# Kernel optimization log

Hardware: AMD Instinct MI355X
Metric: run time of the kernel (lower is better)

The kernel has to match this reference:

```python
import jax, jax.numpy as jnp
import numpy as np

D = 4096
B = 2
S = 2048


def setup_inputs() -> dict:
    key = jax.random.key(0)
    k1, k2, k3, k4 = jax.random.split(key, 4)
    x = jax.random.normal(k1, (B, S, D), dtype=jnp.float32)
    # 2-bit symmetric quantized codes stored as uint8 in torch; torch's
    # clamp(-1,1).to(uint8) wraps -1 -> 255, so codes span {0,1,255}-like
    # values. We draw the full uint8 range for a representative baseline.
    q_int = jax.random.randint(k2, (D, D), 0, 256, dtype=jnp.int32)
    # per-channel positive scales (small, like 2-bit scales: |w|max / 1)
    scale = jax.random.uniform(k3, (D,), dtype=jnp.float32) * 0.01 + 1e-4
    # symmetric quantization -> zero_point = 0 per channel (int buffer)
    zero_point = jnp.zeros((D,), dtype=jnp.int32)
    bias = jax.random.normal(k4, (D,), dtype=jnp.float32) * 0.02
    return {"x": x, "q_int": q_int, "scale": scale,
            "zero_point": zero_point, "bias": bias}


def reference(x, q_int, scale, zero_point, bias):
    # Faithful to FFQLinear.forward:
    #   weight = (q_int.float() - zero_point) * scale
    # NOTE: no unsqueeze(-1) here (unlike pack time), so scale/zp broadcast
    # over the LAST (column) axis of the [d, d] code matrix.
    zp = zero_point.astype(jnp.float32)
    W = (q_int.astype(jnp.float32) - zp[None, :]) * scale[None, :]  # [D, D]
    b, s, d = x.shape
    # F.linear(x2d, W.t(), bias) == x2d @ W + bias
    out = jnp.einsum('bsd,dk->bsk', x, W) + bias  # [B, S, D]
    return out
```

## Files before the change

kernel.cpp:

```cpp
#include <hip/hip_runtime.h>
#include <stdint.h>

typedef unsigned short u16;
typedef __attribute__((ext_vector_type(8))) short short8;
typedef __attribute__((ext_vector_type(4))) float f32x4;

#define KD 4096

typedef const __attribute__((address_space(1))) void* gas1_t;
typedef __attribute__((address_space(3))) void* las3_t;

__device__ __forceinline__ void g2l16(const void* g, void* l) {
  __builtin_amdgcn_global_load_lds((gas1_t)g, (las3_t)l, 16, 0, 0);
}

__device__ __forceinline__ u16 f2bf(float f) {
  uint32_t u = __float_as_uint(f);
  return (u16)((u + 0x7FFFu + ((u >> 16) & 1u)) >> 16);
}

__global__ void cvt_x(const float4* __restrict__ x, uint2* __restrict__ xb) {
  int gid = blockIdx.x * 256 + threadIdx.x;
  float4 f = x[gid];
  union { u16 u[4]; uint2 v; } o;
  o.u[0] = f2bf(f.x); o.u[1] = f2bf(f.y);
  o.u[2] = f2bf(f.z); o.u[3] = f2bf(f.w);
  xb[gid] = o.v;
}

__global__ void cvt_q(const int* __restrict__ q, const int* __restrict__ zp,
                      u16* __restrict__ qt) {
  __shared__ u16 Lt[64][66];
  const int n0 = blockIdx.x * 64;
  const int k0 = blockIdx.y * 64;
  const int nc = threadIdx.x & 15;
  const int kr = threadIdx.x >> 4;

  int z[4];
#pragma unroll
  for (int c = 0; c < 4; ++c) z[c] = zp[n0 + nc * 4 + c];

#pragma unroll
  for (int p = 0; p < 4; ++p) {
    int k = p * 16 + kr;
    int4 v = *(const int4*)(q + (int64_t)(k0 + k) * KD + n0 + nc * 4);
    Lt[k][nc * 4 + 0] = f2bf((float)(v.x - z[0]));
    Lt[k][nc * 4 + 1] = f2bf((float)(v.y - z[1]));
    Lt[k][nc * 4 + 2] = f2bf((float)(v.z - z[2]));
    Lt[k][nc * 4 + 3] = f2bf((float)(v.w - z[3]));
  }
  __syncthreads();

  const int kq = threadIdx.x & 7;
  const int nn = threadIdx.x >> 3;
#pragma unroll
  for (int p = 0; p < 2; ++p) {
    int n = nn + p * 32;
    union { u16 u[8]; uint4 v; } o;
#pragma unroll
    for (int i = 0; i < 8; ++i) o.u[i] = Lt[kq * 8 + i][n];
    *(uint4*)(qt + (int64_t)(n0 + n) * KD + k0 + kq * 8) = o.v;
  }
}

__global__ __launch_bounds__(512, 2)
void gemm8(const u16* __restrict__ A, const u16* __restrict__ Bt,
           const float* __restrict__ scale, const float* __restrict__ bias,
           float* __restrict__ C) {
  __shared__ u16 lds[65536];

  const int tid = threadIdx.x;
  const int orig = blockIdx.x;
  const int lid = (orig & 7) * 32 + (orig >> 3);
  const int bm0 = (lid >> 4) * 256;
  const int bn0 = (lid & 15) * 256;

  const int lane = tid & 63;
  const int w = tid >> 6;
  const int wr = w >> 2;
  const int wc = w & 3;
  const int l15 = lane & 15;
  const int q4 = lane >> 4;
  const int l7 = l15 & 7;

  const int rl = tid >> 3;
  const int csw = (tid & 7) ^ (rl & 7);
  const u16* gA = A + (int64_t)(bm0 + rl) * KD + csw * 8;
  const u16* gB = Bt + (int64_t)(bn0 + rl) * KD + csw * 8;

#define STA(b, qq, kt) g2l16(gA + (int64_t)(qq) * 64 * KD + (kt), &lds[(b) * 32768 + (qq) * 4096 + tid * 8])
#define STB(b, qq, kt) g2l16(gB + (int64_t)(qq) * 64 * KD + (kt), &lds[16384 + (b) * 32768 + (qq) * 4096 + tid * 8])

#define RD_A(mh)                                                              \
  do {                                                                        \
    _Pragma("unroll") for (int m = 0; m < 4; ++m) {                           \
      const int row = wr * 128 + (mh) * 64 + m * 16 + l15;                    \
      _Pragma("unroll") for (int kk = 0; kk < 2; ++kk)                        \
        ar[m][kk] = *(const short8*)&Ab[row * 64 + (((kk * 4 + q4) ^ l7) * 8)]; \
    }                                                                         \
  } while (0)

#define RD_B(nn0)                                                             \
  do {                                                                        \
    _Pragma("unroll") for (int n = 0; n < 2; ++n) {                           \
      const int col = wc * 64 + ((nn0) + n) * 16 + l15;                       \
      _Pragma("unroll") for (int kk = 0; kk < 2; ++kk)                        \
        br[(nn0) + n][kk] = *(const short8*)&Bb[col * 64 + (((kk * 4 + q4) ^ l7) * 8)]; \
    }                                                                         \
  } while (0)

#define MFMA_Q(mb, nn0)                                                       \
  do {                                                                        \
    __builtin_amdgcn_s_setprio(1);                                            \
    _Pragma("unroll") for (int m = 0; m < 4; ++m)                             \
      _Pragma("unroll") for (int n = 0; n < 2; ++n)                           \
        _Pragma("unroll") for (int kk = 0; kk < 2; ++kk)                      \
          acc[(mb) + m][(nn0) + n] = __builtin_amdgcn_mfma_f32_16x16x32_bf16( \
              ar[m][kk], br[(nn0) + n][kk], acc[(mb) + m][(nn0) + n], 0, 0, 0); \
    __builtin_amdgcn_s_setprio(0);                                            \
  } while (0)

#define LGKM0 asm volatile("s_waitcnt lgkmcnt(0)" ::: "memory")
#define BAR __builtin_amdgcn_s_barrier()

  f32x4 acc[8][4];
#pragma unroll
  for (int m = 0; m < 8; ++m)
#pragma unroll
    for (int n = 0; n < 4; ++n) acc[m][n] = (f32x4)(0.f);

  short8 ar[4][2], br[4][2];

  STB(0, 0, 0); STB(0, 1, 0); STB(0, 2, 0); STB(0, 3, 0);
  STA(0, 0, 0); STA(0, 2, 0); STA(0, 1, 0); STA(0, 3, 0);
  asm volatile("s_waitcnt vmcnt(2)" ::: "memory");
  BAR;

  int cur = 0;
  for (int t = 0; t < 63; ++t) {
    const int ktn = (t + 1) * 64;
    const u16* __restrict__ Ab = &lds[cur * 32768];
    const u16* __restrict__ Bb = &lds[16384 + cur * 32768];
    const int nb = cur ^ 1;

    RD_A(0);
    RD_B(0);
    STB(nb, 0, ktn); STB(nb, 1, ktn);
    BAR; LGKM0;
    MFMA_Q(0, 0);
    BAR;

    RD_B(2);
    STB(nb, 2, ktn); STB(nb, 3, ktn);
    asm volatile("s_waitcnt vmcnt(4)" ::: "memory");
    BAR; LGKM0;
    MFMA_Q(0, 2);
    BAR;

    RD_A(1);
    STA(nb, 0, ktn); STA(nb, 2, ktn);
    BAR; LGKM0;
    MFMA_Q(4, 0);
    BAR;

    STA(nb, 1, ktn); STA(nb, 3, ktn);
    asm volatile("s_waitcnt vmcnt(2)" ::: "memory");
    BAR; LGKM0;
    MFMA_Q(4, 2);
    BAR;

    cur ^= 1;
  }

  {
    const u16* __restrict__ Ab = &lds[cur * 32768];
    const u16* __restrict__ Bb = &lds[16384 + cur * 32768];
    RD_A(0);
    RD_B(0);
    BAR; LGKM0;
    MFMA_Q(0, 0);
    BAR;

    RD_B(2);
    asm volatile("s_waitcnt vmcnt(0)" ::: "memory");
    BAR; LGKM0;
    MFMA_Q(0, 2);
    BAR;

    RD_A(1);
    BAR; LGKM0;
    MFMA_Q(4, 0);
    BAR;

    MFMA_Q(4, 2);
  }

  const int r4 = q4 * 4;
#pragma unroll
  for (int n = 0; n < 4; ++n) {
    const int col = bn0 + wc * 64 + n * 16 + l15;
    const float sc = scale[col];
    const float bs = bias[col];
#pragma unroll
    for (int mi = 0; mi < 8; ++mi) {
      const int row = bm0 + wr * 128 + mi * 16 + r4;
#pragma unroll
      for (int j = 0; j < 4; ++j)
        C[(int64_t)(row + j) * KD + col] = acc[mi][n][j] * sc + bs;
    }
  }
}

extern "C" void kernel_launch(void* const* d_in, const int* in_sizes, int n_in,
                              void* d_out, int out_size, void* d_ws, size_t ws_size,
                              hipStream_t stream) {
  const float* x = (const float*)d_in[0];
  const int* q = (const int*)d_in[1];
  const float* scale = (const float*)d_in[2];
  const int* zp = (const int*)d_in[3];
  const float* bias = (const float*)d_in[4];
  float* out = (float*)d_out;

  u16* Xb = (u16*)d_ws;
  u16* Qt = Xb + (size_t)4096 * 4096;

  cvt_x<<<16384, 256, 0, stream>>>((const float4*)x, (uint2*)Xb);

  dim3 gq(4096 / 64, 4096 / 64);
  cvt_q<<<gq, 256, 0, stream>>>(q, zp, Qt);

  gemm8<<<256, 512, 0, stream>>>(Xb, Qt, scale, bias, out);
}
```

Baseline: 294.9 us.

## Fuse conversion kernels and simplify GEMM loop to two barriers per k-step

The two preprocessing kernels (x to bf16, and the transpose-convert of the quantized weights) are merged into one launch. Block ranges select the role, and the weight transpose now packs pairs of k rows into 32-bit LDS words so the readback needs fewer LDS reads. In the GEMM main loop all eight global-to-LDS prefetches for the next tile are issued at once behind a single barrier pair, replacing the four sub-phases that each had barriers. This cuts synchronisation and launch overhead. The trade-offs are coarser overlap between loads and MFMAs and a dependence on the vmcnt(8) accounting being correct.

```diff
diff --git a/kernel.cpp b/kernel.cpp
--- a/kernel.cpp
+++ b/kernel.cpp
@@ -19,35 +19,42 @@
   return (u16)((u + 0x7FFFu + ((u >> 16) & 1u)) >> 16);
 }
 
-__global__ void cvt_x(const float4* __restrict__ x, uint2* __restrict__ xb) {
-  int gid = blockIdx.x * 256 + threadIdx.x;
-  float4 f = x[gid];
-  union { u16 u[4]; uint2 v; } o;
-  o.u[0] = f2bf(f.x); o.u[1] = f2bf(f.y);
-  o.u[2] = f2bf(f.z); o.u[3] = f2bf(f.w);
-  xb[gid] = o.v;
-}
-
-__global__ void cvt_q(const int* __restrict__ q, const int* __restrict__ zp,
-                      u16* __restrict__ qt) {
-  __shared__ u16 Lt[64][66];
-  const int n0 = blockIdx.x * 64;
-  const int k0 = blockIdx.y * 64;
+__global__ __launch_bounds__(256)
+void cvt_fused(const float4* __restrict__ x, const int* __restrict__ q,
+               const int* __restrict__ zp, uint2* __restrict__ xb,
+               u16* __restrict__ qt) {
+  const int b = blockIdx.x;
+  if (b >= 4096) {
+    int gid = (b - 4096) * 256 + threadIdx.x;
+    float4 f = x[gid];
+    union { u16 u[4]; uint2 v; } o;
+    o.u[0] = f2bf(f.x); o.u[1] = f2bf(f.y);
+    o.u[2] = f2bf(f.z); o.u[3] = f2bf(f.w);
+    xb[gid] = o.v;
+    return;
+  }
+  __shared__ uint32_t P[32][68];
+  const int n0 = (b & 63) * 64;
+  const int k0 = (b >> 6) * 64;
   const int nc = threadIdx.x & 15;
   const int kr = threadIdx.x >> 4;
 
   int z[4];
 #pragma unroll
-  for (int c = 0; c < 4; ++c) z[c] = zp[n0 + nc * 4 + c];
-
-#pragma unroll
-  for (int p = 0; p < 4; ++p) {
-    int k = p * 16 + kr;
-    int4 v = *(const int4*)(q + (int64_t)(k0 + k) * KD + n0 + nc * 4);
-    Lt[k][nc * 4 + 0] = f2bf((float)(v.x - z[0]));
-    Lt[k][nc * 4 + 1] = f2bf((float)(v.y - z[1]));
-    Lt[k][nc * 4 + 2] = f2bf((float)(v.z - z[2]));
-    Lt[k][nc * 4 + 3] = f2bf((float)(v.w - z[3]));
+  for (int j = 0; j < 4; ++j) z[j] = zp[n0 + nc * 4 + j];
+
+#pragma unroll
+  for (int s = 0; s < 2; ++s) {
+    const int kp = kr + s * 16;
+    const int64_t rb = (int64_t)(k0 + kp * 2) * KD + n0 + nc * 4;
+    int4 r0 = *(const int4*)(q + rb);
+    int4 r1 = *(const int4*)(q + rb + KD);
+    uint4 w;
+    w.x = (uint32_t)f2bf((float)(r0.x - z[0])) | ((uint32_t)f2bf((float)(r1.x - z[0])) << 16);
+    w.y = (uint32_t)f2bf((float)(r0.y - z[1])) | ((uint32_t)f2bf((float)(r1.y - z[1])) << 16);
+    w.z = (uint32_t)f2bf((float)(r0.z - z[2])) | ((uint32_t)f2bf((float)(r1.z - z[2])) << 16);
+    w.w = (uint32_t)f2bf((float)(r0.w - z[3])) | ((uint32_t)f2bf((float)(r1.w - z[3])) << 16);
+    *(uint4*)&P[kp][nc * 4] = w;
   }
   __syncthreads();
 
@@ -55,11 +62,13 @@
   const int nn = threadIdx.x >> 3;
 #pragma unroll
   for (int p = 0; p < 2; ++p) {
-    int n = nn + p * 32;
-    union { u16 u[8]; uint4 v; } o;
-#pragma unroll
-    for (int i = 0; i < 8; ++i) o.u[i] = Lt[kq * 8 + i][n];
-    *(uint4*)(qt + (int64_t)(n0 + n) * KD + k0 + kq * 8) = o.v;
+    const int n = nn + p * 32;
+    uint4 v;
+    v.x = P[kq * 4 + 0][n];
+    v.y = P[kq * 4 + 1][n];
+    v.z = P[kq * 4 + 2][n];
+    v.w = P[kq * 4 + 3][n];
+    *(uint4*)(qt + (int64_t)(n0 + n) * KD + k0 + kq * 8) = v;
   }
 }
 
@@ -88,8 +97,8 @@
   const u16* gA = A + (int64_t)(bm0 + rl) * KD + csw * 8;
   const u16* gB = Bt + (int64_t)(bn0 + rl) * KD + csw * 8;
 
-#define STA(b, qq, kt) g2l16(gA + (int64_t)(qq) * 64 * KD + (kt), &lds[(b) * 32768 + (qq) * 4096 + tid * 8])
-#define STB(b, qq, kt) g2l16(gB + (int64_t)(qq) * 64 * KD + (kt), &lds[16384 + (b) * 32768 + (qq) * 4096 + tid * 8])
+#define STA(b_, qq, kt) g2l16(gA + (int64_t)(qq) * 64 * KD + (kt), &lds[(b_) * 32768 + (qq) * 4096 + tid * 8])
+#define STB(b_, qq, kt) g2l16(gB + (int64_t)(qq) * 64 * KD + (kt), &lds[16384 + (b_) * 32768 + (qq) * 4096 + tid * 8])
 
 #define RD_A(mh)                                                              \
   do {                                                                        \
@@ -120,8 +129,11 @@
     __builtin_amdgcn_s_setprio(0);                                            \
   } while (0)
 
-#define LGKM0 asm volatile("s_waitcnt lgkmcnt(0)" ::: "memory")
 #define BAR __builtin_amdgcn_s_barrier()
+#define SCHED0 __builtin_amdgcn_sched_barrier(0)
+#define CFENCE asm volatile("" ::: "memory")
+#define VMC8 asm volatile("s_waitcnt vmcnt(8)" ::: "memory")
+#define VMC0 asm volatile("s_waitcnt vmcnt(0)" ::: "memory")
 
   f32x4 acc[8][4];
 #pragma unroll
@@ -132,9 +144,7 @@
   short8 ar[4][2], br[4][2];
 
   STB(0, 0, 0); STB(0, 1, 0); STB(0, 2, 0); STB(0, 3, 0);
-  STA(0, 0, 0); STA(0, 2, 0); STA(0, 1, 0); STA(0, 3, 0);
-  asm volatile("s_waitcnt vmcnt(2)" ::: "memory");
-  BAR;
+  STA(0, 0, 0); STA(0, 1, 0); STA(0, 2, 0); STA(0, 3, 0);
 
   int cur = 0;
   for (int t = 0; t < 63; ++t) {
@@ -143,31 +153,22 @@
     const u16* __restrict__ Bb = &lds[16384 + cur * 32768];
     const int nb = cur ^ 1;
 
+    SCHED0; CFENCE;
+    BAR;
+    STB(nb, 0, ktn); STB(nb, 1, ktn); STB(nb, 2, ktn); STB(nb, 3, ktn);
+    STA(nb, 0, ktn); STA(nb, 1, ktn); STA(nb, 2, ktn); STA(nb, 3, ktn);
+    VMC8;
+    BAR;
+    SCHED0; CFENCE;
+
     RD_A(0);
     RD_B(0);
-    STB(nb, 0, ktn); STB(nb, 1, ktn);
-    BAR; LGKM0;
+    RD_B(2);
     MFMA_Q(0, 0);
-    BAR;
-
-    RD_B(2);
-    STB(nb, 2, ktn); STB(nb, 3, ktn);
-    asm volatile("s_waitcnt vmcnt(4)" ::: "memory");
-    BAR; LGKM0;
     MFMA_Q(0, 2);
-    BAR;
-
     RD_A(1);
-    STA(nb, 0, ktn); STA(nb, 2, ktn);
-    BAR; LGKM0;
     MFMA_Q(4, 0);
-    BAR;
-
-    STA(nb, 1, ktn); STA(nb, 3, ktn);
-    asm volatile("s_waitcnt vmcnt(2)" ::: "memory");
-    BAR; LGKM0;
     MFMA_Q(4, 2);
-    BAR;
 
     cur ^= 1;
   }
@@ -175,23 +176,18 @@
   {
     const u16* __restrict__ Ab = &lds[cur * 32768];
     const u16* __restrict__ Bb = &lds[16384 + cur * 32768];
+    SCHED0; CFENCE;
+    BAR;
+    VMC0;
+    BAR;
+    SCHED0; CFENCE;
     RD_A(0);
     RD_B(0);
-    BAR; LGKM0;
+    RD_B(2);
     MFMA_Q(0, 0);
-    BAR;
-
-    RD_B(2);
-    asm volatile("s_waitcnt vmcnt(0)" ::: "memory");
-    BAR; LGKM0;
     MFMA_Q(0, 2);
-    BAR;
-
     RD_A(1);
-    BAR; LGKM0;
     MFMA_Q(4, 0);
-    BAR;
-
     MFMA_Q(4, 2);
   }
 
@@ -224,10 +220,8 @@
   u16* Xb = (u16*)d_ws;
   u16* Qt = Xb + (size_t)4096 * 4096;
 
-  cvt_x<<<16384, 256, 0, stream>>>((const float4*)x, (uint2*)Xb);
-
-  dim3 gq(4096 / 64, 4096 / 64);
-  cvt_q<<<gq, 256, 0, stream>>>(q, zp, Qt);
+  cvt_fused<<<20480, 256, 0, stream>>>((const float4*)x, q, zp,
+                                       (uint2*)Xb, Qt);
 
   gemm8<<<256, 512, 0, stream>>>(Xb, Qt, scale, bias, out);
 }
```

Result: faster. 288.0 us (-2.3%).
